# Performance work log

Hardware: AMD Instinct MI355X
Metric: run time of the kernel (lower is better)

## Reference

```python
import jax, jax.numpy as jnp
import numpy as np

B, C, H, W = 8, 512, 64, 64
D = C // 8  # 64

def setup_inputs() -> dict:
    key = jax.random.key(0)
    ks = jax.random.split(key, 10)
    s = 0.02
    return {
        "x":  jax.random.normal(ks[0], (B, C, H, W), dtype=jnp.float32),
        "Wq": jax.random.normal(ks[1], (D, C), dtype=jnp.float32) * s,
        "bq": jnp.zeros((D,), dtype=jnp.float32),
        "Wk": jax.random.normal(ks[2], (D, C), dtype=jnp.float32) * s,
        "bk": jnp.zeros((D,), dtype=jnp.float32),
        "Wv": jax.random.normal(ks[3], (D, C), dtype=jnp.float32) * s,
        "bv": jnp.zeros((D,), dtype=jnp.float32),
        "Wo": jax.random.normal(ks[4], (C, D), dtype=jnp.float32) * s,
        "bo": jnp.zeros((C,), dtype=jnp.float32),
        "gamma": jnp.full((1,), 0.5, dtype=jnp.float32),
    }

def reference(x, Wq, bq, Wk, bk, Wv, bv, Wo, bo, gamma):
    b, c, h, w = x.shape
    n = h * w
    xf = x.reshape(b, c, n)                                   # (B, C, N)
    # 1x1 convs == channel matmuls (spectral_norm only reparametrizes the weight)
    q = jnp.einsum('dc,bcn->bnd', Wq, xf) + bq                # (B, N, D)
    k = jnp.einsum('dc,bcn->bdn', Wk, xf) + bk[:, None]       # (B, D, N)
    v = jnp.einsum('dc,bcn->bdn', Wv, xf) + bv[:, None]       # (B, D, N)
    # unscaled scores, softmax over key index (last dim)
    attn = jax.nn.softmax(jnp.einsum('bnd,bdm->bnm', q, k), axis=-1)  # (B, N, N)
    out = jnp.einsum('bdm,bnm->bdn', v, attn)                 # (B, D, N)
    out = jnp.einsum('cd,bdn->bcn', Wo, out) + bo[:, None]    # (B, C, N)
    return (out * gamma + xf).reshape(b, c, h, w)
```

## Files before the change

kernel.cpp:

```cpp
#include <hip/hip_runtime.h>
#include <hip/hip_bf16.h>

#define DEVFN __device__ __forceinline__

typedef __bf16 bf16x8 __attribute__((ext_vector_type(8)));
typedef float f32x4 __attribute__((ext_vector_type(4)));
typedef float float4_t __attribute__((ext_vector_type(4)));
typedef unsigned short ushort8_t __attribute__((ext_vector_type(8)));
typedef unsigned short ushort4_t __attribute__((ext_vector_type(4)));
typedef unsigned int uint4_t __attribute__((ext_vector_type(4)));

constexpr int Bd = 8, Cd = 512, Nd = 4096, Dd = 64;

DEVFN unsigned short f2bf(float f) {
    union { float f; unsigned int u; } v; v.f = f;
    unsigned int r = (v.u + 0x7FFFu + ((v.u >> 16) & 1u)) >> 16;
    return (unsigned short)r;
}

DEVFN unsigned int pack2(float a, float b) {
    __hip_bfloat162 h = __float22bfloat162_rn(make_float2(a, b));
    union { __hip_bfloat162 h; unsigned int u; } c; c.h = h;
    return c.u;
}

DEVFN bf16x8 ld_bf8(const unsigned short* p) {
    ushort8_t u = *(const ushort8_t*)p;
    return __builtin_bit_cast(bf16x8, u);
}

DEVFN f32x4 mfma16(bf16x8 a, bf16x8 b, f32x4 c) {
    return __builtin_amdgcn_mfma_f32_16x16x32_bf16(a, b, c, 0, 0, 0);
}

__global__ __launch_bounds__(256) void k_cvtw(
    const float* __restrict__ Wq, const float* __restrict__ Wk,
    const float* __restrict__ Wv, const float* __restrict__ Wo,
    unsigned short* __restrict__ w4)
{
    int i = blockIdx.x * 256 + threadIdx.x;
    w4[i]          = f2bf(Wq[i]);
    w4[32768 + i]  = f2bf(Wk[i]);
    w4[65536 + i]  = f2bf(Wv[i]);
    w4[98304 + i]  = f2bf(Wo[i]);
}

__global__ __launch_bounds__(128, 2) void k_qkv(
    const float* __restrict__ x,
    const unsigned short* __restrict__ wq,
    const unsigned short* __restrict__ wk,
    const unsigned short* __restrict__ wv,
    const float* __restrict__ bq, const float* __restrict__ bk, const float* __restrict__ bv,
    unsigned short* __restrict__ q_nd, unsigned short* __restrict__ k_nd,
    unsigned short* __restrict__ v_dn)
{
    const int b   = blockIdx.y;
    const int n0  = blockIdx.x * 32;
    const int tid = threadIdx.x, wid = tid >> 6, l = tid & 63;
    const int lo  = l & 15, hi = l >> 4;
    const float* xb = x + (size_t)b * Cd * Nd;

    __shared__ unsigned short smem[2][32][72];

    f32x4 acc[12] = {};

    const int scr = tid >> 3;
    const int snf = tid & 7;
    float4_t xrA[4], xrB[4];

    auto gloadA = [&](int t) {
        const int c0 = t * 64;
        #pragma unroll
        for (int p = 0; p < 4; ++p)
            xrA[p] = *(const float4_t*)(xb + (size_t)(c0 + p*16 + scr) * Nd + n0 + snf*4);
    };
    auto gloadB = [&](int t) {
        const int c0 = t * 64;
        #pragma unroll
        for (int p = 0; p < 4; ++p)
            xrB[p] = *(const float4_t*)(xb + (size_t)(c0 + p*16 + scr) * Nd + n0 + snf*4);
    };
    auto dswriteA = [&](int buf) {
        #pragma unroll
        for (int p = 0; p < 4; ++p)
            #pragma unroll
            for (int i = 0; i < 4; ++i)
                smem[buf][snf*4 + i][p*16 + scr] = f2bf(xrA[p][i]);
    };
    auto dswriteB = [&](int buf) {
        #pragma unroll
        for (int p = 0; p < 4; ++p)
            #pragma unroll
            for (int i = 0; i < 4; ++i)
                smem[buf][snf*4 + i][p*16 + scr] = f2bf(xrB[p][i]);
    };
    auto compute = [&](int buf, int t) {
        const int c0 = t * 64;
        #pragma unroll
        for (int kk = 0; kk < 2; ++kk) {
            bf16x8 af = ld_bf8(&smem[buf][wid*16 + lo][kk*32 + hi*8]);
            #pragma unroll
            for (int j = 0; j < 12; ++j) {
                const unsigned short* wm = (j < 4) ? wq : (j < 8) ? wk : wv;
                const int d0 = (j & 3) * 16;
                bf16x8 bf = ld_bf8(wm + (d0 + lo) * Cd + c0 + kk*32 + hi*8);
                acc[j] = mfma16(af, bf, acc[j]);
            }
        }
    };

    gloadA(0);
    dswriteA(0);
    gloadB(1);
    __syncthreads();
    for (int t = 0; t < 8; t += 2) {
        if (t + 2 < 8) gloadA(t + 2);
        __builtin_amdgcn_sched_barrier(0);
        compute(0, t);
        dswriteB(1);
        __syncthreads();
        if (t + 3 < 8) gloadB(t + 3);
        __builtin_amdgcn_sched_barrier(0);
        compute(1, t + 1);
        if (t + 2 < 8) dswriteA(0);
        __syncthreads();
    }

    unsigned short* tl = &smem[1][wid*16][0];
    #pragma unroll
    for (int m = 0; m < 2; ++m) {
        const float* bias = m ? bk : bq;
        #pragma unroll
        for (int jj = 0; jj < 4; ++jj) {
            const float bia = bias[jj*16 + lo];
            #pragma unroll
            for (int r = 0; r < 4; ++r)
                tl[(hi*4 + r) * 72 + jj*16 + lo] = f2bf(acc[m*4 + jj][r] + bia);
        }
        asm volatile("" ::: "memory");
        const int row = l >> 2, dg = l & 3;
        ushort8_t a0 = *(const ushort8_t*)&tl[row*72 + dg*16];
        ushort8_t a1 = *(const ushort8_t*)&tl[row*72 + dg*16 + 8];
        unsigned short* dst = (m ? k_nd : q_nd)
            + ((size_t)b * Nd + n0 + wid*16 + row) * 64 + dg*16;
        *(ushort8_t*)dst = a0; *(ushort8_t*)(dst + 8) = a1;
        asm volatile("" ::: "memory");
    }

    unsigned short* vt = &smem[0][0][0];
    #pragma unroll
    for (int jj = 0; jj < 4; ++jj) {
        const float bia = bv[jj*16 + lo];
        #pragma unroll
        for (int r = 0; r < 4; ++r)
            vt[(jj*16 + lo) * 36 + wid*16 + hi*4 + r] = f2bf(acc[8 + jj][r] + bia);
    }
    __syncthreads();
    #pragma unroll
    for (int p = 0; p < 2; ++p) {
        const int d = p*32 + (tid >> 2), ng = tid & 3;
        ushort4_t a0 = *(const ushort4_t*)&vt[d*36 + ng*8];
        ushort4_t a1 = *(const ushort4_t*)&vt[d*36 + ng*8 + 4];
        unsigned short* dst = v_dn + ((size_t)b * Dd + d) * Nd + n0 + ng*8;
        *(ushort4_t*)dst = a0; *(ushort4_t*)(dst + 4) = a1;
    }
}

__global__ __launch_bounds__(512, 4) void k_attn(
    const unsigned short* __restrict__ q_nd,
    const unsigned short* __restrict__ k_nd,
    const unsigned short* __restrict__ v_dn,
    unsigned short* __restrict__ o_nd)
{
    const int bid = blockIdx.x;
    const int b   = bid & 7;
    const int n0  = (bid >> 3) * 64;
    const int tid = threadIdx.x, wid = tid >> 6, l = tid & 63;
    const int lo  = l & 15, hi = l >> 4;
    const int lsw = lo & 7;
    const int qh  = wid >> 2;
    const int kh  = (wid >> 1) & 1;
    const int tp  = wid & 1;
    const int wk0 = kh * 32;

    __shared__ __align__(16) unsigned short kv_lds[2][2][2][64 * 64];
    __shared__ float red_l[3][2][2][16];

    const unsigned short* qb = q_nd + (size_t)b * Nd * Dd;
    const unsigned short* kb = k_nd + (size_t)b * Nd * Dd;
    const unsigned short* vb = v_dn + (size_t)b * Dd * Nd;

    bf16x8 aq[2][2];
    #pragma unroll
    for (int qs = 0; qs < 2; ++qs)
        #pragma unroll
        for (int kc = 0; kc < 2; ++kc)
            aq[qs][kc] = ld_bf8(qb + (size_t)(n0 + qh*32 + qs*16 + lo) * 64 + kc*32 + hi*8);

    f32x4 acc[2][4] = {};
    float l_p[2] = {0.f, 0.f};

    const int sr = tid >> 3, ss = tid & 7;
    const int kwsl = (ss ^ (sr & 7)) * 8;
    const int vkh = ss >> 2, vsl = ss & 3, vms = vsl >> 1;
    const int vg0 = vkh * 4 + ((2 * vsl) & 3);
    const int vg1 = vkh * 4 + ((2 * vsl + 1) & 3);
    const int vsw = sr & 7;
    ushort8_t kr0, kr1, vr0, vr1;

    auto gload = [&](int it) {
        const size_t m1 = (size_t)it * 128;
        kr0 = *(const ushort8_t*)(kb + (m1 + sr) * 64 + ss * 8);
        kr1 = *(const ushort8_t*)(kb + (m1 + 64 + sr) * 64 + ss * 8);
        vr0 = *(const ushort8_t*)(vb + (size_t)sr * Nd + m1 + ss * 8);
        vr1 = *(const ushort8_t*)(vb + (size_t)sr * Nd + m1 + 64 + ss * 8);
    };
    auto dswrite = [&](int buf) {
        unsigned short* kt0 = &kv_lds[0][buf][0][0];
        unsigned short* kt1 = &kv_lds[0][buf][1][0];
        unsigned short* vt0 = &kv_lds[1][buf][0][0];
        unsigned short* vt1 = &kv_lds[1][buf][1][0];
        *(ushort8_t*)(kt0 + sr * 64 + kwsl) = kr0;
        *(ushort8_t*)(kt1 + sr * 64 + kwsl) = kr1;
        ushort4_t a0 = __builtin_shufflevector(vr0, vr0, 0, 1, 2, 3);
        ushort4_t a1 = __builtin_shufflevector(vr0, vr0, 4, 5, 6, 7);
        ushort4_t b0 = __builtin_shufflevector(vr1, vr1, 0, 1, 2, 3);
        ushort4_t b1 = __builtin_shufflevector(vr1, vr1, 4, 5, 6, 7);
        *(ushort4_t*)(vt0 + sr * 64 + (vg0 ^ vsw) * 8 + vms * 4) = a0;
        *(ushort4_t*)(vt0 + sr * 64 + (vg1 ^ vsw) * 8 + vms * 4) = a1;
        *(ushort4_t*)(vt1 + sr * 64 + (vg0 ^ vsw) * 8 + vms * 4) = b0;
        *(ushort4_t*)(vt1 + sr * 64 + (vg1 ^ vsw) * 8 + vms * 4) = b1;
    };

    auto compute = [&](int buf) {
        const unsigned short* kt = &kv_lds[0][buf][tp][0];
        const unsigned short* vt = &kv_lds[1][buf][tp][0];
        f32x4 s[2][2] = {};
        #pragma unroll
        for (int ms = 0; ms < 2; ++ms) {
            #pragma unroll
            for (int kc = 0; kc < 2; ++kc) {
                bf16x8 kf = ld_bf8(kt + (wk0 + ms*16 + lo) * 64 + (((kc*4 + hi) ^ lsw) * 8));
                #pragma unroll
                for (int qs = 0; qs < 2; ++qs)
                    s[qs][ms] = mfma16(kf, aq[qs][kc], s[qs][ms]);
            }
        }
        bf16x8 vf[4];
        #pragma unroll
        for (int ds = 0; ds < 4; ++ds)
            vf[ds] = ld_bf8(vt + (ds*16 + lo) * 64 + (((kh*4 + hi) ^ lsw) * 8));
        #pragma unroll
        for (int qs = 0; qs < 2; ++qs) {
            float p[2][4];
            #pragma unroll
            for (int ms = 0; ms < 2; ++ms)
                #pragma unroll
                for (int r = 0; r < 4; ++r)
                    p[ms][r] = __expf(s[qs][ms][r]);
            l_p[qs] += ((p[0][0] + p[0][1]) + (p[0][2] + p[0][3]))
                     + ((p[1][0] + p[1][1]) + (p[1][2] + p[1][3]));
            uint4_t w;
            w[0] = pack2(p[0][0], p[0][1]);
            w[1] = pack2(p[0][2], p[0][3]);
            w[2] = pack2(p[1][0], p[1][1]);
            w[3] = pack2(p[1][2], p[1][3]);
            bf16x8 apf = __builtin_bit_cast(bf16x8, w);
            #pragma unroll
            for (int ds = 0; ds < 4; ++ds)
                acc[qs][ds] = mfma16(apf, vf[ds], acc[qs][ds]);
        }
    };

    constexpr int NIT = Nd / 128;
    gload(0);
    dswrite(0);
    __syncthreads();
    for (int it = 0; it < NIT; ++it) {
        const int cur = it & 1;
        if (it + 1 < NIT) gload(it + 1);
        __builtin_amdgcn_sched_barrier(0);
        compute(cur);
        if (it + 1 < NIT) dswrite(cur ^ 1);
        __syncthreads();
    }

    float lh[2];
    #pragma unroll
    for (int qs = 0; qs < 2; ++qs) {
        float ps = l_p[qs];
        ps += __shfl_xor(ps, 16, 64);
        ps += __shfl_xor(ps, 32, 64);
        lh[qs] = ps;
    }
    float* red = (float*)&kv_lds[0][0][0][0];
    const int g = (kh * 2 + tp) - 1;
    if (g >= 0) {
        #pragma unroll
        for (int qs = 0; qs < 2; ++qs) {
            #pragma unroll
            for (int ds = 0; ds < 4; ++ds) {
                const int idx = ((g * 2 + qh) * 2 + qs) * 4 + ds;
                *(f32x4*)&red[idx * 256 + l * 4] = acc[qs][ds];
            }
            red_l[g][qh][qs][lo] = lh[qs];
        }
    }
    __syncthreads();
    if (g < 0) {
        #pragma unroll
        for (int qs = 0; qs < 2; ++qs) {
            #pragma unroll
            for (int gg = 0; gg < 3; ++gg) {
                #pragma unroll
                for (int ds = 0; ds < 4; ++ds) {
                    const int idx = ((gg * 2 + qh) * 2 + qs) * 4 + ds;
                    acc[qs][ds] += *(const f32x4*)&red[idx * 256 + l * 4];
                }
                lh[qs] += red_l[gg][qh][qs][lo];
            }
            #pragma unroll
            for (int r = 0; r < 4; ++r) {
                float lq = __shfl(lh[qs], hi * 4 + r, 16);
                float rl = 1.0f / lq;
                #pragma unroll
                for (int ds = 0; ds < 4; ++ds) {
                    float o = acc[qs][ds][r] * rl;
                    o_nd[((size_t)b * Nd + n0 + qh*32 + qs*16 + hi*4 + r) * 64 + ds*16 + lo] = f2bf(o);
                }
            }
        }
    }
}

__global__ __launch_bounds__(256) void k_oproj(
    const unsigned short* __restrict__ o_nd,
    const unsigned short* __restrict__ wo,
    const float* __restrict__ bo,
    const float* __restrict__ gamma,
    const float* __restrict__ x,
    float* __restrict__ out)
{
    const int b   = blockIdx.y;
    const int n0  = blockIdx.x * 64;
    const int tid = threadIdx.x, wid = tid >> 6, l = tid & 63;
    const int lo  = l & 15, hi = l >> 4;
    const int n0w = n0 + wid * 16;
    const float g = gamma[0];

    bf16x8 ao[2];
    #pragma unroll
    for (int kc = 0; kc < 2; ++kc)
        ao[kc] = ld_bf8(o_nd + ((size_t)b * Nd + n0w + lo) * 64 + kc*32 + hi*8);

    for (int ct = 0; ct < 32; ++ct) {
        f32x4 acc = {};
        #pragma unroll
        for (int kc = 0; kc < 2; ++kc) {
            bf16x8 bw = ld_bf8(wo + (ct*16 + lo) * 64 + kc*32 + hi*8);
            acc = mfma16(ao[kc], bw, acc);
        }
        const int c = ct*16 + lo;
        const float bc = bo[c];
        const size_t base = ((size_t)b * Cd + c) * Nd + n0w + hi*4;
        float4_t xv = *(const float4_t*)(x + base);
        float4_t ov;
        #pragma unroll
        for (int r = 0; r < 4; ++r) ov[r] = g * (acc[r] + bc) + xv[r];
        *(float4_t*)(out + base) = ov;
    }
}

extern "C" void kernel_launch(void* const* d_in, const int* in_sizes, int n_in,
                              void* d_out, int out_size, void* d_ws, size_t ws_size,
                              hipStream_t stream) {
    (void)in_sizes; (void)n_in; (void)out_size; (void)ws_size;
    const float* x  = (const float*)d_in[0];
    const float* Wq = (const float*)d_in[1];
    const float* bq = (const float*)d_in[2];
    const float* Wk = (const float*)d_in[3];
    const float* bk = (const float*)d_in[4];
    const float* Wv = (const float*)d_in[5];
    const float* bv = (const float*)d_in[6];
    const float* Wo = (const float*)d_in[7];
    const float* bo = (const float*)d_in[8];
    const float* gm = (const float*)d_in[9];
    float* out = (float*)d_out;

    unsigned short* w4   = (unsigned short*)d_ws;
    unsigned short* q_nd = w4 + 131072;
    unsigned short* k_nd = q_nd + (size_t)Bd * Nd * Dd;
    unsigned short* v_dn = k_nd + (size_t)Bd * Nd * Dd;
    unsigned short* o_nd = v_dn + (size_t)Bd * Nd * Dd;

    k_cvtw<<<128, 256, 0, stream>>>(Wq, Wk, Wv, Wo, w4);
    dim3 gq(Nd / 32, Bd);
    k_qkv<<<gq, 128, 0, stream>>>(x, w4, w4 + 32768, w4 + 65536, bq, bk, bv, q_nd, k_nd, v_dn);
    k_attn<<<512, 512, 0, stream>>>(q_nd, k_nd, v_dn, o_nd);
    dim3 g1(Nd / 64, Bd);
    k_oproj<<<g1, 256, 0, stream>>>(o_nd, w4 + 98304, bo, gm, x, out);
}
```

Baseline: 142.5 us.

## Enlarge QKV projection tile to 128 positions with 8 waves and swizzled LDS

The QKV projection kernel now handles 128 spatial positions per block with 512 threads instead of 32 positions with 128 threads. The x tile is stored in LDS in channel-major order with an XOR swizzle, written as vectorized 4-wide rows, and read back as strided per-element gathers to form MFMA A fragments. The aim is wider coalesced global loads of x, fewer blocks, and more reuse of each weight fragment across waves. The costs are a scalar 8-element LDS gather per fragment, fewer blocks in the grid (256) for the GPU to spread across CUs, and an extra barrier in the epilogue.

```diff
diff --git a/kernel.cpp b/kernel.cpp
--- a/kernel.cpp
+++ b/kernel.cpp
@@ -45,7 +45,7 @@
     w4[98304 + i]  = f2bf(Wo[i]);
 }
 
-__global__ __launch_bounds__(128, 2) void k_qkv(
+__global__ __launch_bounds__(512, 2) void k_qkv(
     const float* __restrict__ x,
     const unsigned short* __restrict__ wq,
     const unsigned short* __restrict__ wk,
@@ -55,56 +55,67 @@
     unsigned short* __restrict__ v_dn)
 {
     const int b   = blockIdx.y;
-    const int n0  = blockIdx.x * 32;
+    const int n0  = blockIdx.x * 128;
     const int tid = threadIdx.x, wid = tid >> 6, l = tid & 63;
     const int lo  = l & 15, hi = l >> 4;
     const float* xb = x + (size_t)b * Cd * Nd;
 
-    __shared__ unsigned short smem[2][32][72];
+    __shared__ __align__(16) unsigned short sm[2][64][136];
 
     f32x4 acc[12] = {};
 
-    const int scr = tid >> 3;
-    const int snf = tid & 7;
+    const int lrow = l >> 5;
+    const int lcol = (l & 31) * 4;
     float4_t xrA[4], xrB[4];
 
     auto gloadA = [&](int t) {
         const int c0 = t * 64;
         #pragma unroll
-        for (int p = 0; p < 4; ++p)
-            xrA[p] = *(const float4_t*)(xb + (size_t)(c0 + p*16 + scr) * Nd + n0 + snf*4);
+        for (int i = 0; i < 4; ++i)
+            xrA[i] = *(const float4_t*)(xb + (size_t)(c0 + wid*8 + lrow + i*2) * Nd + n0 + lcol);
     };
     auto gloadB = [&](int t) {
         const int c0 = t * 64;
         #pragma unroll
-        for (int p = 0; p < 4; ++p)
-            xrB[p] = *(const float4_t*)(xb + (size_t)(c0 + p*16 + scr) * Nd + n0 + snf*4);
-    };
+        for (int i = 0; i < 4; ++i)
+            xrB[i] = *(const float4_t*)(xb + (size_t)(c0 + wid*8 + lrow + i*2) * Nd + n0 + lcol);
+    };
+    const int wswz = (wid & 3) * 8;
     auto dswriteA = [&](int buf) {
         #pragma unroll
-        for (int p = 0; p < 4; ++p)
-            #pragma unroll
-            for (int i = 0; i < 4; ++i)
-                smem[buf][snf*4 + i][p*16 + scr] = f2bf(xrA[p][i]);
+        for (int i = 0; i < 4; ++i) {
+            const int rl = wid*8 + lrow + i*2;
+            ushort4_t u;
+            #pragma unroll
+            for (int j = 0; j < 4; ++j) u[j] = f2bf(xrA[i][j]);
+            *(ushort4_t*)&sm[buf][rl][lcol ^ wswz] = u;
+        }
     };
     auto dswriteB = [&](int buf) {
         #pragma unroll
-        for (int p = 0; p < 4; ++p)
-            #pragma unroll
-            for (int i = 0; i < 4; ++i)
-                smem[buf][snf*4 + i][p*16 + scr] = f2bf(xrB[p][i]);
+        for (int i = 0; i < 4; ++i) {
+            const int rl = wid*8 + lrow + i*2;
+            ushort4_t u;
+            #pragma unroll
+            for (int j = 0; j < 4; ++j) u[j] = f2bf(xrB[i][j]);
+            *(ushort4_t*)&sm[buf][rl][lcol ^ wswz] = u;
+        }
     };
     auto compute = [&](int buf, int t) {
-        const int c0 = t * 64;
         #pragma unroll
         for (int kk = 0; kk < 2; ++kk) {
-            bf16x8 af = ld_bf8(&smem[buf][wid*16 + lo][kk*32 + hi*8]);
-            #pragma unroll
-            for (int j = 0; j < 12; ++j) {
-                const unsigned short* wm = (j < 4) ? wq : (j < 8) ? wk : wv;
-                const int d0 = (j & 3) * 16;
-                bf16x8 bf = ld_bf8(wm + (d0 + lo) * Cd + c0 + kk*32 + hi*8);
-                acc[j] = mfma16(af, bf, acc[j]);
+            const int rc = (wid*16 + lo) ^ (hi*8);
+            ushort8_t ua;
+            #pragma unroll
+            for (int j = 0; j < 8; ++j)
+                ua[j] = sm[buf][kk*32 + hi*8 + j][rc];
+            bf16x8 af = __builtin_bit_cast(bf16x8, ua);
+            #pragma unroll
+            for (int jj = 0; jj < 12; ++jj) {
+                const unsigned short* wm = (jj < 4) ? wq : (jj < 8) ? wk : wv;
+                const int d0 = (jj & 3) * 16;
+                bf16x8 bf = ld_bf8(wm + (d0 + lo) * Cd + t*64 + kk*32 + hi*8);
+                acc[jj] = mfma16(af, bf, acc[jj]);
             }
         }
     };
@@ -126,7 +137,8 @@
         __syncthreads();
     }
 
-    unsigned short* tl = &smem[1][wid*16][0];
+    unsigned short* epi = &sm[0][0][0];
+    unsigned short* tl  = epi + wid * 16 * 72;
     #pragma unroll
     for (int m = 0; m < 2; ++m) {
         const float* bias = m ? bk : bq;
@@ -146,23 +158,23 @@
         *(ushort8_t*)dst = a0; *(ushort8_t*)(dst + 8) = a1;
         asm volatile("" ::: "memory");
     }
-
-    unsigned short* vt = &smem[0][0][0];
+    __syncthreads();
+
+    unsigned short* vt2 = &sm[0][0][0];
     #pragma unroll
     for (int jj = 0; jj < 4; ++jj) {
         const float bia = bv[jj*16 + lo];
         #pragma unroll
         for (int r = 0; r < 4; ++r)
-            vt[(jj*16 + lo) * 36 + wid*16 + hi*4 + r] = f2bf(acc[8 + jj][r] + bia);
+            vt2[(jj*16 + lo) * 136 + wid*16 + hi*4 + r] = f2bf(acc[8 + jj][r] + bia);
     }
     __syncthreads();
-    #pragma unroll
-    for (int p = 0; p < 2; ++p) {
-        const int d = p*32 + (tid >> 2), ng = tid & 3;
-        ushort4_t a0 = *(const ushort4_t*)&vt[d*36 + ng*8];
-        ushort4_t a1 = *(const ushort4_t*)&vt[d*36 + ng*8 + 4];
-        unsigned short* dst = v_dn + ((size_t)b * Dd + d) * Nd + n0 + ng*8;
-        *(ushort4_t*)dst = a0; *(ushort4_t*)(dst + 4) = a1;
+    {
+        const int d = tid >> 3, nc = (tid & 7) * 16;
+        ushort8_t a0 = *(const ushort8_t*)&vt2[d*136 + nc];
+        ushort8_t a1 = *(const ushort8_t*)&vt2[d*136 + nc + 8];
+        unsigned short* dst = v_dn + ((size_t)b * Dd + d) * Nd + n0 + nc;
+        *(ushort8_t*)dst = a0; *(ushort8_t*)(dst + 8) = a1;
     }
 }
 
@@ -394,8 +406,8 @@
     unsigned short* o_nd = v_dn + (size_t)Bd * Nd * Dd;
 
     k_cvtw<<<128, 256, 0, stream>>>(Wq, Wk, Wv, Wo, w4);
-    dim3 gq(Nd / 32, Bd);
-    k_qkv<<<gq, 128, 0, stream>>>(x, w4, w4 + 32768, w4 + 65536, bq, bk, bv, q_nd, k_nd, v_dn);
+    dim3 gq(Nd / 128, Bd);
+    k_qkv<<<gq, 512, 0, stream>>>(x, w4, w4 + 32768, w4 + 65536, bq, bk, bv, q_nd, k_nd, v_dn);
     k_attn<<<512, 512, 0, stream>>>(q_nd, k_nd, v_dn, o_nd);
     dim3 g1(Nd / 64, Bd);
     k_oproj<<<g1, 256, 0, stream>>>(o_nd, w4 + 98304, bo, gm, x, out);
```

Measured after the change: 147.5 us. 3.6% more time.
